# Kernel tuning notes

Measured on AMD Instinct MI355X. Metric: run time of the kernel, lower is better.

The kernel has to match this reference:

```python
import jax, jax.numpy as jnp
import numpy as np

N_NODES = 100000


def gcn_conv(x, edge_index, W, b):
    # PyG GCNConv: add self-loops, symmetric normalization D^-1/2 (A+I) D^-1/2, transform, aggregate, bias.
    src, dst = edge_index[0], edge_index[1]
    n = x.shape[0]
    xw = x @ W  # [N, out] transform before propagate (PyG order)
    # degree with self-loops (count edges by target + 1)
    deg = jax.ops.segment_sum(jnp.ones_like(dst, dtype=xw.dtype), dst, num_segments=n) + 1.0
    dinv = jax.lax.rsqrt(deg)  # deg >= 1, safe
    norm = dinv[src] * dinv[dst]  # [E]
    msgs = xw[src] * norm[:, None]  # [E, out] gathered, normalized messages
    agg = jax.ops.segment_sum(msgs, dst, num_segments=n)
    # self-loop contribution: norm_ii = dinv_i^2 = 1/deg_i
    agg = agg + xw * (dinv * dinv)[:, None]
    return agg + b


def setup_inputs() -> dict:
    key = jax.random.key(0)
    ks = jax.random.split(key, 8)
    in_c, h1, h2, out_c = 128, 71, 82, 1
    x = jax.random.normal(ks[0], (N_NODES, in_c), dtype=jnp.float32)
    edge_index = jax.random.randint(ks[1], (2, 1600000), 0, N_NODES, dtype=jnp.int64)
    def glorot(k, fan_in, fan_out):
        s = jnp.sqrt(6.0 / (fan_in + fan_out))
        return jax.random.uniform(k, (fan_in, fan_out), jnp.float32, -s, s)
    return {
        "x": x,
        "edge_index": edge_index,
        "W1": glorot(ks[2], in_c, h1), "b1": jnp.zeros((h1,), jnp.float32),
        "W2": glorot(ks[3], h1, h2), "b2": jnp.zeros((h2,), jnp.float32),
        "W3": glorot(ks[4], h2, out_c), "b3": jnp.zeros((out_c,), jnp.float32),
    }


def reference(x, edge_index, W1, b1, W2, b2, W3, b3):
    h = jax.nn.relu(gcn_conv(x, edge_index, W1, b1))
    h = gcn_conv(h, edge_index, W2, b2)  # note: no relu after conv2 in source
    return gcn_conv(h, edge_index, W3, b3)
```

## Files before the change

### kernel.cpp

```cpp
#include <hip/hip_runtime.h>
#include <hip/hip_fp16.h>

#define NNODES 100000
#define NB 196
#define BSHIFT 9
#define BMASK 511
#define BCAP 9216
#define WT_LD 136

typedef _Float16 half8 __attribute__((ext_vector_type(8)));
typedef float floatx4 __attribute__((ext_vector_type(4)));

__global__ void binA_kernel(const int* __restrict__ src, const int* __restrict__ dst,
                            int* __restrict__ bcnt, unsigned* __restrict__ bdata, int E) {
    __shared__ int hist[NB];
    __shared__ int gb[NB];
    __shared__ int cur[NB];
    const int BATCH = 4096;
    for (int base = blockIdx.x * BATCH; base < E; base += gridDim.x * BATCH) {
        for (int i = threadIdx.x; i < NB; i += blockDim.x) hist[i] = 0;
        __syncthreads();
        int s[16], d[16];
        int cnt = 0;
        if (base + BATCH <= E) {
#pragma unroll
            for (int q = 0; q < 4; ++q) {
                int4 sv = ((const int4*)(src + base))[q * 256 + threadIdx.x];
                int4 dv = ((const int4*)(dst + base))[q * 256 + threadIdx.x];
                s[cnt] = sv.x; d[cnt] = dv.x; atomicAdd(&hist[dv.x >> BSHIFT], 1); ++cnt;
                s[cnt] = sv.y; d[cnt] = dv.y; atomicAdd(&hist[dv.y >> BSHIFT], 1); ++cnt;
                s[cnt] = sv.z; d[cnt] = dv.z; atomicAdd(&hist[dv.z >> BSHIFT], 1); ++cnt;
                s[cnt] = sv.w; d[cnt] = dv.w; atomicAdd(&hist[dv.w >> BSHIFT], 1); ++cnt;
            }
        } else {
#pragma unroll
            for (int k = 0; k < 16; ++k) {
                int idx = base + k * 256 + threadIdx.x;
                if (idx < E) {
                    s[cnt] = src[idx];
                    d[cnt] = dst[idx];
                    atomicAdd(&hist[d[cnt] >> BSHIFT], 1);
                    ++cnt;
                }
            }
        }
        __syncthreads();
        for (int i = threadIdx.x; i < NB; i += blockDim.x) {
            int c = hist[i];
            gb[i] = (c > 0) ? atomicAdd(&bcnt[i], c) : 0;
            cur[i] = 0;
        }
        __syncthreads();
        for (int k = 0; k < cnt; ++k) {
            int b = d[k] >> BSHIFT;
            int lo = gb[b] + atomicAdd(&cur[b], 1);
            if (lo < BCAP)
                bdata[(size_t)b * BCAP + lo] = ((unsigned)s[k] << BSHIFT) | ((unsigned)d[k] & BMASK);
        }
        __syncthreads();
    }
}

__global__ __launch_bounds__(1024) void prep_kernel(
        const int* __restrict__ bcnt, int* __restrict__ bstart,
        const float* __restrict__ W2, const float* __restrict__ b2,
        const float* __restrict__ W3, float* __restrict__ w23,
        const float* __restrict__ W1, __half* __restrict__ Wt) {
    if (blockIdx.x == 0) {
        __shared__ int sh[NB];
        int t = threadIdx.x;
        if (t < NB) sh[t] = min(bcnt[t], BCAP);
        __syncthreads();
        if (t == 0) {
            int acc = 0;
            for (int i = 0; i < NB; ++i) { int v = sh[i]; sh[i] = acc; acc += v; }
        }
        __syncthreads();
        if (t < NB) bstart[t] = sh[t];
    } else if (blockIdx.x == 1) {
        int k = threadIdx.x;
        if (k < 71) {
            float a = 0.f;
            for (int j = 0; j < 82; ++j) a += W2[k * 82 + j] * W3[j];
            w23[k] = a;
        } else if (k == 71) {
            float a = 0.f;
            for (int j = 0; j < 82; ++j) a += b2[j] * W3[j];
            w23[71] = a;
        }
    } else {
        for (int i = threadIdx.x; i < 80 * WT_LD; i += blockDim.x) {
            int nn = i / WT_LD, k = i - nn * WT_LD;
            float v = (nn < 71 && k < 128) ? W1[k * 71 + nn] : 0.f;
            Wt[i] = __float2half(v);
        }
    }
}

__global__ __launch_bounds__(1024) void binB2_kernel(
        const int* __restrict__ bcnt, const int* __restrict__ bstart,
        const unsigned* __restrict__ bdata,
        int* __restrict__ deg, int* __restrict__ end_off, float* __restrict__ dinv,
        int* __restrict__ csr, int n) {
    __shared__ unsigned edata[BCAP];
    __shared__ int hist[512];
    __shared__ int cur[512];
    __shared__ int wsum[8];
    int b = blockIdx.x;
    int tid = threadIdx.x;
    int cnt = min(bcnt[b], BCAP);
    int base = bstart[b];
    const unsigned* p = bdata + (size_t)b * BCAP;
    if (tid < 512) hist[tid] = 0;
    __syncthreads();
    for (int i = tid; i < cnt; i += 1024) {
        unsigned e = p[i];
        edata[i] = e;
        atomicAdd(&hist[e & BMASK], 1);
    }
    __syncthreads();
    if (tid < 512) {
        int v = hist[tid];
        int lane = tid & 63;
        int incl = v;
#pragma unroll
        for (int off = 1; off < 64; off <<= 1) {
            int t = __shfl_up(incl, off);
            if (lane >= off) incl += t;
        }
        cur[tid] = incl;
        if (lane == 63) wsum[tid >> 6] = incl;
    }
    __syncthreads();
    if (tid == 0) {
        int acc = 0;
#pragma unroll
        for (int w = 0; w < 8; ++w) { int t = wsum[w]; wsum[w] = acc; acc += t; }
    }
    __syncthreads();
    if (tid < 512) {
        int v = hist[tid];
        int start = base + wsum[tid >> 6] + cur[tid] - v;
        int node = (b << BSHIFT) + tid;
        if (node < n) {
            deg[node] = v;
            end_off[node] = start + v;
            dinv[node] = rsqrtf((float)v + 1.0f);
        }
        cur[tid] = start;
    }
    __syncthreads();
    for (int i = tid; i < cnt; i += 1024) {
        unsigned e = edata[i];
        int pos = atomicAdd(&cur[e & BMASK], 1);
        csr[pos] = (int)(e >> BSHIFT);
    }
}

__global__ __launch_bounds__(256) void xform_mfma(
        const float* __restrict__ x, const __half* __restrict__ Wt,
        const float* __restrict__ scale, __half* __restrict__ msgA,
        __half* __restrict__ msgB, int n) {
    __shared__ __half Wsh[80 * WT_LD];
    {
        const uint4* sp = (const uint4*)Wt;
        uint4* dp = (uint4*)Wsh;
        for (int i = threadIdx.x; i < (80 * WT_LD * 2) / 16; i += blockDim.x) dp[i] = sp[i];
    }
    __syncthreads();
    int lane = threadIdx.x & 63;
    int m = lane & 15, q = lane >> 4;
    int gw = (blockIdx.x * blockDim.x + threadIdx.x) >> 6;
    int nw = (gridDim.x * blockDim.x) >> 6;
    int nrt = n >> 4;
    for (int rt = gw; rt < nrt; rt += nw) {
        int rb = rt << 4;
        const float* xr = x + (size_t)(rb + m) * 128 + q * 8;
        floatx4 acc[5];
#pragma unroll
        for (int t = 0; t < 5; ++t) acc[t] = (floatx4){0.f, 0.f, 0.f, 0.f};
#pragma unroll
        for (int ks = 0; ks < 4; ++ks) {
            float4 f0 = *(const float4*)(xr + ks * 32);
            float4 f1 = *(const float4*)(xr + ks * 32 + 4);
            half8 a;
            a[0] = (_Float16)f0.x; a[1] = (_Float16)f0.y;
            a[2] = (_Float16)f0.z; a[3] = (_Float16)f0.w;
            a[4] = (_Float16)f1.x; a[5] = (_Float16)f1.y;
            a[6] = (_Float16)f1.z; a[7] = (_Float16)f1.w;
#pragma unroll
            for (int t = 0; t < 5; ++t) {
                half8 b = *(const half8*)&Wsh[(t * 16 + m) * WT_LD + ks * 32 + q * 8];
                acc[t] = __builtin_amdgcn_mfma_f32_16x16x32_f16(a, b, acc[t], 0, 0, 0);
            }
        }
        float sc[4];
#pragma unroll
        for (int r = 0; r < 4; ++r) sc[r] = scale[rb + q * 4 + r];
#pragma unroll
        for (int t = 0; t < 5; ++t) {
            int col = t * 16 + m;
#pragma unroll
            for (int r = 0; r < 4; ++r) {
                __half hv = __float2half(acc[t][r] * sc[r]);
                int row = rb + q * 4 + r;
                if (t < 4) {
                    msgA[(size_t)row * 64 + col] = hv;
                } else if (m < 8) {
                    msgB[(size_t)row * 8 + m] = hv;
                }
            }
        }
    }
}

__global__ __launch_bounds__(256) void gather_fused(
        const __half* __restrict__ msgA, const __half* __restrict__ msgB,
        const int* __restrict__ csr, const int* __restrict__ end_off,
        const int* __restrict__ deg, const float* __restrict__ dinv,
        const float* __restrict__ b, const float* __restrict__ w23,
        float* __restrict__ g2, int n) {
    int lane = threadIdx.x & 63;
    int li = lane & 7;
    int wid = (blockIdx.x * blockDim.x + threadIdx.x) >> 6;
    int nwaves = (gridDim.x * blockDim.x) >> 6;
    float bA[8], wA[8];
#pragma unroll
    for (int j = 0; j < 8; ++j) { bA[j] = b[8 * li + j]; wA[j] = w23[8 * li + j]; }
    float bB = (li < 7) ? b[64 + li] : 0.f;
    float wB = (li < 7) ? w23[64 + li] : 0.f;
    const char* mA = (const char*)msgA;
    const char* mB = (const char*)msgB;
    unsigned laneA   = (unsigned)(li << 4);
    unsigned laneBof = (unsigned)((li >> 1) << 2);
    unsigned laneBsh = (unsigned)((li & 1) << 4);
    int ntiles = (n + 7) >> 3;
    for (int tile = wid; tile < ntiles; tile += nwaves) {
        int node = (tile << 3) + (lane >> 3);
        int d = -1, st = 0; float dv = 0.f;
        if (node < n) {
            int e = end_off[node];
            d = deg[node];
            st = e - d;
            dv = dinv[node];
        }
        int tmax = d;
        tmax = max(tmax, __shfl_xor(tmax, 8));
        tmax = max(tmax, __shfl_xor(tmax, 16));
        tmax = max(tmax, __shfl_xor(tmax, 32));
        tmax = __builtin_amdgcn_readfirstlane(tmax);
        float acc[8];
#pragma unroll
        for (int j = 0; j < 8; ++j) acc[j] = 0.f;
        float bsum = 0.f;
        int c0 = csr[(0 < d) ? st : 0];
        int c1 = csr[(1 < d) ? st + 1 : 0];
        for (int i = 0; i <= tmax; i += 2) {
            int p0 = csr[(i + 2 < d) ? st + i + 2 : 0];
            int p1 = csr[(i + 3 < d) ? st + i + 3 : 0];
            if (i <= d) {
                unsigned idx = (unsigned)((i < d) ? c0 : node);
                half8 row = *(const half8*)(mA + ((idx << 7) | laneA));
                unsigned bw = *(const unsigned*)(mB + ((idx << 4) | laneBof));
#pragma unroll
                for (int j = 0; j < 8; ++j) acc[j] += (float)row[j];
                unsigned short us = (unsigned short)(bw >> laneBsh);
                _Float16 hf;
                __builtin_memcpy(&hf, &us, 2);
                bsum += (float)hf;
            }
            if (i + 1 <= d) {
                unsigned idx = (unsigned)((i + 1 < d) ? c1 : node);
                half8 row = *(const half8*)(mA + ((idx << 7) | laneA));
                unsigned bw = *(const unsigned*)(mB + ((idx << 4) | laneBof));
#pragma unroll
                for (int j = 0; j < 8; ++j) acc[j] += (float)row[j];
                unsigned short us = (unsigned short)(bw >> laneBsh);
                _Float16 hf;
                __builtin_memcpy(&hf, &us, 2);
                bsum += (float)hf;
            }
            c0 = p0;
            c1 = p1;
        }
        float p = 0.f;
#pragma unroll
        for (int j = 0; j < 8; ++j) p += fmaxf(dv * acc[j] + bA[j], 0.f) * wA[j];
        p += fmaxf(dv * bsum + bB, 0.f) * wB;
        p += __shfl_xor(p, 1);
        p += __shfl_xor(p, 2);
        p += __shfl_xor(p, 4);
        if (node < n && li == 0) g2[node] = dv * p;
    }
}

__global__ void sgather_q(const float* __restrict__ g2, const int* __restrict__ csr,
                          const int* __restrict__ end_off, const int* __restrict__ deg,
                          const float* __restrict__ dinv, const float* __restrict__ w23,
                          float* __restrict__ q, int n) {
    float bw = w23[71];
    int lane = threadIdx.x & 63;
    int g = lane >> 4, k = lane & 15;
    int wid = (blockIdx.x * blockDim.x + threadIdx.x) >> 6;
    int nw = (gridDim.x * blockDim.x) >> 6;
    for (int i0 = wid * 4; i0 < n; i0 += nw * 4) {
        int i = i0 + g;
        float acc = 0.f;
        float dv = 0.f;
        if (i < n) {
            int end = end_off[i];
            int cnt = deg[i];
            int start = end - cnt;
            dv = dinv[i];
            for (int e = k; e < cnt; e += 16) acc += g2[csr[start + e]];
        }
        acc += __shfl_down(acc, 8, 16);
        acc += __shfl_down(acc, 4, 16);
        acc += __shfl_down(acc, 2, 16);
        acc += __shfl_down(acc, 1, 16);
        if (i < n && k == 0) q[i] = dv * (dv * (acc + g2[i]) + bw);
    }
}

__global__ void sgather_out(const float* __restrict__ q, const int* __restrict__ csr,
                            const int* __restrict__ end_off, const int* __restrict__ deg,
                            const float* __restrict__ dinv, const float* __restrict__ b3,
                            float* __restrict__ out, int n) {
    float bv = b3[0];
    int lane = threadIdx.x & 63;
    int g = lane >> 4, k = lane & 15;
    int wid = (blockIdx.x * blockDim.x + threadIdx.x) >> 6;
    int nw = (gridDim.x * blockDim.x) >> 6;
    for (int i0 = wid * 4; i0 < n; i0 += nw * 4) {
        int i = i0 + g;
        float acc = 0.f;
        float dv = 0.f;
        if (i < n) {
            int end = end_off[i];
            int cnt = deg[i];
            int start = end - cnt;
            dv = dinv[i];
            for (int e = k; e < cnt; e += 16) acc += q[csr[start + e]];
        }
        acc += __shfl_down(acc, 8, 16);
        acc += __shfl_down(acc, 4, 16);
        acc += __shfl_down(acc, 2, 16);
        acc += __shfl_down(acc, 1, 16);
        if (i < n && k == 0) out[i] = dv * (acc + q[i]) + bv;
    }
}

extern "C" void kernel_launch(void* const* d_in, const int* in_sizes, int n_in,
                              void* d_out, int out_size, void* d_ws, size_t ws_size,
                              hipStream_t stream) {
    const float* x  = (const float*)d_in[0];
    const int*   ei = (const int*)d_in[1];
    const float* W1 = (const float*)d_in[2];
    const float* b1 = (const float*)d_in[3];
    const float* W2 = (const float*)d_in[4];
    const float* b2 = (const float*)d_in[5];
    const float* W3 = (const float*)d_in[6];
    const float* b3 = (const float*)d_in[7];
    float* out = (float*)d_out;

    const int n = NNODES;
    const int E = in_sizes[1] / 2;
    const int* src = ei;
    const int* dst = ei + E;

    float* ws     = (float*)d_ws;
    float* dinv   = ws;
    int*   deg_i  = (int*)(ws + n);
    int*   offs   = deg_i + n;
    int*   bcnt   = offs + n;
    int*   bstart = bcnt + 256;
    float* w23    = (float*)(bstart + 256);
    __half* Wt    = (__half*)(w23 + 80);
    float* g2     = (float*)(Wt + 11008);
    float* q      = g2 + n;
    int*   csr    = (int*)(q + n);
    __half* msgA  = (__half*)(csr + E + 16);
    __half* msgB  = msgA + (size_t)n * 64;
    unsigned* bdata = (unsigned*)(msgB + (size_t)n * 8);

    hipMemsetAsync(bcnt, 0, 256 * sizeof(int), stream);
    binA_kernel<<<(E + 4095) / 4096, 256, 0, stream>>>(src, dst, bcnt, bdata, E);
    prep_kernel<<<3, 1024, 0, stream>>>(bcnt, bstart, W2, b2, W3, w23, W1, Wt);
    binB2_kernel<<<NB, 1024, 0, stream>>>(bcnt, bstart, bdata, deg_i, offs, dinv, csr, n);

    xform_mfma<<<1563, 256, 0, stream>>>(x, Wt, dinv, msgA, msgB, n);

    gather_fused<<<1563, 256, 0, stream>>>(msgA, msgB, csr, offs, deg_i, dinv, b1, w23, g2, n);

    sgather_q<<<1024, 256, 0, stream>>>(g2, csr, offs, deg_i, dinv, w23, q, n);
    sgather_out<<<1024, 256, 0, stream>>>(q, csr, offs, deg_i, dinv, b3, out, n);
}
```

Before: 225.7 us.

## Software-pipeline layer-1 gather with fdot2 accumulation, finer bins, larger grids

The layer-1 gather now keeps 16 outstanding row loads in flight with explicit double-buffered issue/consume stages and scheduling barriers. It accumulates half pairs via fdot2 and uses a zero sentinel row instead of per-edge predication. Binning switches to 256-node buckets across more blocks, the scalar gathers unroll by two, and grids double. These are meant to hide gather latency and raise parallelism, at the cost of higher register pressure and extra padded iterations for low-degree tiles.

```diff
diff --git a/kernel.cpp b/kernel.cpp
--- a/kernel.cpp
+++ b/kernel.cpp
@@ -2,13 +2,14 @@
 #include <hip/hip_fp16.h>
 
 #define NNODES 100000
-#define NB 196
-#define BSHIFT 9
-#define BMASK 511
-#define BCAP 9216
+#define NB 391
+#define BSHIFT 8
+#define BMASK 255
+#define BCAP 4864
 #define WT_LD 136
 
 typedef _Float16 half8 __attribute__((ext_vector_type(8)));
+typedef _Float16 half2_t __attribute__((ext_vector_type(2)));
 typedef float floatx4 __attribute__((ext_vector_type(4)));
 
 __global__ void binA_kernel(const int* __restrict__ src, const int* __restrict__ dst,
@@ -103,15 +104,15 @@
         int* __restrict__ deg, int* __restrict__ end_off, float* __restrict__ dinv,
         int* __restrict__ csr, int n) {
     __shared__ unsigned edata[BCAP];
-    __shared__ int hist[512];
-    __shared__ int cur[512];
-    __shared__ int wsum[8];
+    __shared__ int hist[256];
+    __shared__ int cur[256];
+    __shared__ int wsum[4];
     int b = blockIdx.x;
     int tid = threadIdx.x;
     int cnt = min(bcnt[b], BCAP);
     int base = bstart[b];
     const unsigned* p = bdata + (size_t)b * BCAP;
-    if (tid < 512) hist[tid] = 0;
+    if (tid < 256) hist[tid] = 0;
     __syncthreads();
     for (int i = tid; i < cnt; i += 1024) {
         unsigned e = p[i];
@@ -119,7 +120,7 @@
         atomicAdd(&hist[e & BMASK], 1);
     }
     __syncthreads();
-    if (tid < 512) {
+    if (tid < 256) {
         int v = hist[tid];
         int lane = tid & 63;
         int incl = v;
@@ -135,10 +136,10 @@
     if (tid == 0) {
         int acc = 0;
 #pragma unroll
-        for (int w = 0; w < 8; ++w) { int t = wsum[w]; wsum[w] = acc; acc += t; }
-    }
-    __syncthreads();
-    if (tid < 512) {
+        for (int w = 0; w < 4; ++w) { int t = wsum[w]; wsum[w] = acc; acc += t; }
+    }
+    __syncthreads();
+    if (tid < 256) {
         int v = hist[tid];
         int start = base + wsum[tid >> 6] + cur[tid] - v;
         int node = (b << BSHIFT) + tid;
@@ -214,83 +215,135 @@
     }
 }
 
+
+#define CONS(RR, WW) do { \
+    half2_t p0_ = {RR[0], RR[1]}, p1_ = {RR[2], RR[3]}; \
+    half2_t p2_ = {RR[4], RR[5]}, p3_ = {RR[6], RR[7]}; \
+    a0 = __builtin_amdgcn_fdot2(p0_, H10, a0, false); \
+    a1 = __builtin_amdgcn_fdot2(p0_, H01, a1, false); \
+    a2 = __builtin_amdgcn_fdot2(p1_, H10, a2, false); \
+    a3 = __builtin_amdgcn_fdot2(p1_, H01, a3, false); \
+    a4 = __builtin_amdgcn_fdot2(p2_, H10, a4, false); \
+    a5 = __builtin_amdgcn_fdot2(p2_, H01, a5, false); \
+    a6 = __builtin_amdgcn_fdot2(p3_, H10, a6, false); \
+    a7 = __builtin_amdgcn_fdot2(p3_, H01, a7, false); \
+    half2_t wv_; __builtin_memcpy(&wv_, &(WW), 4); \
+    bsum = __builtin_amdgcn_fdot2(wv_, HB, bsum, false); \
+} while (0)
+
+#define ISSUE(S, C, RR, WW, S2) do { \
+    unsigned idx_ = ((S) < d) ? (unsigned)(C) : ZR; \
+    RR = *(const half8*)(mA + (((size_t)idx_ << 7) | laneA)); \
+    WW = *(const unsigned*)(mB + (((size_t)idx_ << 4) | laneBof)); \
+    C = csr[((S2) < d) ? st + (S2) : 0]; \
+} while (0)
+
+#define PISSUE(S, CV, RR, WW) do { \
+    unsigned idx_ = ((S) < d) ? (unsigned)(CV) : ZR; \
+    RR = *(const half8*)(mA + (((size_t)idx_ << 7) | laneA)); \
+    WW = *(const unsigned*)(mB + (((size_t)idx_ << 4) | laneBof)); \
+} while (0)
+
+#define CSRP(S) csr[((S) < d) ? st + (S) : 0]
+
 __global__ __launch_bounds__(256) void gather_fused(
         const __half* __restrict__ msgA, const __half* __restrict__ msgB,
         const int* __restrict__ csr, const int* __restrict__ end_off,
         const int* __restrict__ deg, const float* __restrict__ dinv,
         const float* __restrict__ b, const float* __restrict__ w23,
         float* __restrict__ g2, int n) {
+    const unsigned ZR = (unsigned)NNODES;
+    const half2_t H10 = {(_Float16)1.f, (_Float16)0.f};
+    const half2_t H01 = {(_Float16)0.f, (_Float16)1.f};
     int lane = threadIdx.x & 63;
     int li = lane & 7;
+    const half2_t HB = (li & 1) ? H01 : H10;
     int wid = (blockIdx.x * blockDim.x + threadIdx.x) >> 6;
     int nwaves = (gridDim.x * blockDim.x) >> 6;
-    float bA[8], wA[8];
-#pragma unroll
-    for (int j = 0; j < 8; ++j) { bA[j] = b[8 * li + j]; wA[j] = w23[8 * li + j]; }
-    float bB = (li < 7) ? b[64 + li] : 0.f;
-    float wB = (li < 7) ? w23[64 + li] : 0.f;
     const char* mA = (const char*)msgA;
     const char* mB = (const char*)msgB;
     unsigned laneA   = (unsigned)(li << 4);
     unsigned laneBof = (unsigned)((li >> 1) << 2);
-    unsigned laneBsh = (unsigned)((li & 1) << 4);
-    int ntiles = (n + 7) >> 3;
+    int ntiles = n >> 3;
     for (int tile = wid; tile < ntiles; tile += nwaves) {
         int node = (tile << 3) + (lane >> 3);
-        int d = -1, st = 0; float dv = 0.f;
-        if (node < n) {
-            int e = end_off[node];
-            d = deg[node];
-            st = e - d;
-            dv = dinv[node];
-        }
+        int ee = end_off[node];
+        int d = deg[node];
+        int st = ee - d;
+        float dv = dinv[node];
         int tmax = d;
         tmax = max(tmax, __shfl_xor(tmax, 8));
         tmax = max(tmax, __shfl_xor(tmax, 16));
         tmax = max(tmax, __shfl_xor(tmax, 32));
         tmax = __builtin_amdgcn_readfirstlane(tmax);
-        float acc[8];
-#pragma unroll
-        for (int j = 0; j < 8; ++j) acc[j] = 0.f;
-        float bsum = 0.f;
-        int c0 = csr[(0 < d) ? st : 0];
-        int c1 = csr[(1 < d) ? st + 1 : 0];
-        for (int i = 0; i <= tmax; i += 2) {
-            int p0 = csr[(i + 2 < d) ? st + i + 2 : 0];
-            int p1 = csr[(i + 3 < d) ? st + i + 3 : 0];
-            if (i <= d) {
-                unsigned idx = (unsigned)((i < d) ? c0 : node);
-                half8 row = *(const half8*)(mA + ((idx << 7) | laneA));
-                unsigned bw = *(const unsigned*)(mB + ((idx << 4) | laneBof));
-#pragma unroll
-                for (int j = 0; j < 8; ++j) acc[j] += (float)row[j];
-                unsigned short us = (unsigned short)(bw >> laneBsh);
-                _Float16 hf;
-                __builtin_memcpy(&hf, &us, 2);
-                bsum += (float)hf;
-            }
-            if (i + 1 <= d) {
-                unsigned idx = (unsigned)((i + 1 < d) ? c1 : node);
-                half8 row = *(const half8*)(mA + ((idx << 7) | laneA));
-                unsigned bw = *(const unsigned*)(mB + ((idx << 4) | laneBof));
-#pragma unroll
-                for (int j = 0; j < 8; ++j) acc[j] += (float)row[j];
-                unsigned short us = (unsigned short)(bw >> laneBsh);
-                _Float16 hf;
-                __builtin_memcpy(&hf, &us, 2);
-                bsum += (float)hf;
-            }
-            c0 = p0;
-            c1 = p1;
-        }
+        int tmaxr = (tmax + 15) & ~15;
+        float a0, a1, a2, a3, a4, a5, a6, a7, bsum;
+        {
+            half8 sr = *(const half8*)(mA + (((size_t)(unsigned)node << 7) | laneA));
+            unsigned sw = *(const unsigned*)(mB + (((size_t)(unsigned)node << 4) | laneBof));
+            a0 = (float)sr[0]; a1 = (float)sr[1]; a2 = (float)sr[2]; a3 = (float)sr[3];
+            a4 = (float)sr[4]; a5 = (float)sr[5]; a6 = (float)sr[6]; a7 = (float)sr[7];
+            half2_t wv; __builtin_memcpy(&wv, &sw, 4);
+            bsum = __builtin_amdgcn_fdot2(wv, HB, 0.f, false);
+        }
+        int k0 = CSRP(0),  k1 = CSRP(1),  k2 = CSRP(2),  k3 = CSRP(3);
+        int k4 = CSRP(4),  k5 = CSRP(5),  k6 = CSRP(6),  k7 = CSRP(7);
+        int k8 = CSRP(8),  k9 = CSRP(9),  k10 = CSRP(10), k11 = CSRP(11);
+        int k12 = CSRP(12), k13 = CSRP(13), k14 = CSRP(14), k15 = CSRP(15);
+        int ca0 = CSRP(16), ca1 = CSRP(17), ca2 = CSRP(18), ca3 = CSRP(19);
+        int ca4 = CSRP(20), ca5 = CSRP(21), ca6 = CSRP(22), ca7 = CSRP(23);
+        int cb0 = CSRP(24), cb1 = CSRP(25), cb2 = CSRP(26), cb3 = CSRP(27);
+        int cb4 = CSRP(28), cb5 = CSRP(29), cb6 = CSRP(30), cb7 = CSRP(31);
+        half8 ra0, ra1, ra2, ra3, ra4, ra5, ra6, ra7;
+        half8 rb0, rb1, rb2, rb3, rb4, rb5, rb6, rb7;
+        unsigned wa0, wa1, wa2, wa3, wa4, wa5, wa6, wa7;
+        unsigned wb0, wb1, wb2, wb3, wb4, wb5, wb6, wb7;
+        PISSUE(0, k0, ra0, wa0);  PISSUE(1, k1, ra1, wa1);
+        PISSUE(2, k2, ra2, wa2);  PISSUE(3, k3, ra3, wa3);
+        PISSUE(4, k4, ra4, wa4);  PISSUE(5, k5, ra5, wa5);
+        PISSUE(6, k6, ra6, wa6);  PISSUE(7, k7, ra7, wa7);
+        PISSUE(8, k8, rb0, wb0);  PISSUE(9, k9, rb1, wb1);
+        PISSUE(10, k10, rb2, wb2); PISSUE(11, k11, rb3, wb3);
+        PISSUE(12, k12, rb4, wb4); PISSUE(13, k13, rb5, wb5);
+        PISSUE(14, k14, rb6, wb6); PISSUE(15, k15, rb7, wb7);
+        for (int i = 0; i < tmaxr; i += 16) {
+            CONS(ra0, wa0); CONS(ra1, wa1); CONS(ra2, wa2); CONS(ra3, wa3);
+            CONS(ra4, wa4); CONS(ra5, wa5); CONS(ra6, wa6); CONS(ra7, wa7);
+            __builtin_amdgcn_sched_barrier(0);
+            ISSUE(i + 16, ca0, ra0, wa0, i + 32);
+            ISSUE(i + 17, ca1, ra1, wa1, i + 33);
+            ISSUE(i + 18, ca2, ra2, wa2, i + 34);
+            ISSUE(i + 19, ca3, ra3, wa3, i + 35);
+            ISSUE(i + 20, ca4, ra4, wa4, i + 36);
+            ISSUE(i + 21, ca5, ra5, wa5, i + 37);
+            ISSUE(i + 22, ca6, ra6, wa6, i + 38);
+            ISSUE(i + 23, ca7, ra7, wa7, i + 39);
+            __builtin_amdgcn_sched_barrier(0);
+            CONS(rb0, wb0); CONS(rb1, wb1); CONS(rb2, wb2); CONS(rb3, wb3);
+            CONS(rb4, wb4); CONS(rb5, wb5); CONS(rb6, wb6); CONS(rb7, wb7);
+            __builtin_amdgcn_sched_barrier(0);
+            ISSUE(i + 24, cb0, rb0, wb0, i + 40);
+            ISSUE(i + 25, cb1, rb1, wb1, i + 41);
+            ISSUE(i + 26, cb2, rb2, wb2, i + 42);
+            ISSUE(i + 27, cb3, rb3, wb3, i + 43);
+            ISSUE(i + 28, cb4, rb4, wb4, i + 44);
+            ISSUE(i + 29, cb5, rb5, wb5, i + 45);
+            ISSUE(i + 30, cb6, rb6, wb6, i + 46);
+            ISSUE(i + 31, cb7, rb7, wb7, i + 47);
+            __builtin_amdgcn_sched_barrier(0);
+        }
+        float av[8] = {a0, a1, a2, a3, a4, a5, a6, a7};
         float p = 0.f;
 #pragma unroll
-        for (int j = 0; j < 8; ++j) p += fmaxf(dv * acc[j] + bA[j], 0.f) * wA[j];
+        for (int j = 0; j < 8; ++j)
+            p += fmaxf(dv * av[j] + b[8 * li + j], 0.f) * w23[8 * li + j];
+        float bB = (li < 7) ? b[64 + li] : 0.f;
+        float wB = (li < 7) ? w23[64 + li] : 0.f;
         p += fmaxf(dv * bsum + bB, 0.f) * wB;
         p += __shfl_xor(p, 1);
         p += __shfl_xor(p, 2);
         p += __shfl_xor(p, 4);
-        if (node < n && li == 0) g2[node] = dv * p;
+        if (li == 0) g2[node] = dv * p;
     }
 }
 
@@ -312,7 +365,13 @@
             int cnt = deg[i];
             int start = end - cnt;
             dv = dinv[i];
-            for (int e = k; e < cnt; e += 16) acc += g2[csr[start + e]];
+            int e = k;
+            for (; e + 16 < cnt; e += 32) {
+                int a0 = csr[start + e];
+                int a1 = csr[start + e + 16];
+                acc += g2[a0] + g2[a1];
+            }
+            for (; e < cnt; e += 16) acc += g2[csr[start + e]];
         }
         acc += __shfl_down(acc, 8, 16);
         acc += __shfl_down(acc, 4, 16);
@@ -340,7 +399,13 @@
             int cnt = deg[i];
             int start = end - cnt;
             dv = dinv[i];
-            for (int e = k; e < cnt; e += 16) acc += q[csr[start + e]];
+            int e = k;
+            for (; e + 16 < cnt; e += 32) {
+                int a0 = csr[start + e];
+                int a1 = csr[start + e + 16];
+                acc += q[a0] + q[a1];
+            }
+            for (; e < cnt; e += 16) acc += q[csr[start + e]];
         }
         acc += __shfl_down(acc, 8, 16);
         acc += __shfl_down(acc, 4, 16);
@@ -373,25 +438,27 @@
     int*   deg_i  = (int*)(ws + n);
     int*   offs   = deg_i + n;
     int*   bcnt   = offs + n;
-    int*   bstart = bcnt + 256;
-    float* w23    = (float*)(bstart + 256);
+    int*   bstart = bcnt + 512;
+    float* w23    = (float*)(bstart + 512);
     __half* Wt    = (__half*)(w23 + 80);
     float* g2     = (float*)(Wt + 11008);
     float* q      = g2 + n;
     int*   csr    = (int*)(q + n);
     __half* msgA  = (__half*)(csr + E + 16);
-    __half* msgB  = msgA + (size_t)n * 64;
-    unsigned* bdata = (unsigned*)(msgB + (size_t)n * 8);
-
-    hipMemsetAsync(bcnt, 0, 256 * sizeof(int), stream);
+    __half* msgB  = msgA + (size_t)(n + 8) * 64;
+    unsigned* bdata = (unsigned*)(msgB + (size_t)(n + 8) * 8);
+
+    hipMemsetAsync(bcnt, 0, 512 * sizeof(int), stream);
+    hipMemsetAsync(msgA + (size_t)n * 64, 0, 64 * sizeof(__half), stream);
+    hipMemsetAsync(msgB + (size_t)n * 8, 0, 8 * sizeof(__half), stream);
     binA_kernel<<<(E + 4095) / 4096, 256, 0, stream>>>(src, dst, bcnt, bdata, E);
     prep_kernel<<<3, 1024, 0, stream>>>(bcnt, bstart, W2, b2, W3, w23, W1, Wt);
     binB2_kernel<<<NB, 1024, 0, stream>>>(bcnt, bstart, bdata, deg_i, offs, dinv, csr, n);
 
     xform_mfma<<<1563, 256, 0, stream>>>(x, Wt, dinv, msgA, msgB, n);
 
-    gather_fused<<<1563, 256, 0, stream>>>(msgA, msgB, csr, offs, deg_i, dinv, b1, w23, g2, n);
-
-    sgather_q<<<1024, 256, 0, stream>>>(g2, csr, offs, deg_i, dinv, w23, q, n);
-    sgather_out<<<1024, 256, 0, stream>>>(q, csr, offs, deg_i, dinv, b3, out, n);
-}
+    gather_fused<<<3125, 256, 0, stream>>>(msgA, msgB, csr, offs, deg_i, dinv, b1, w23, g2, n);
+
+    sgather_q<<<2048, 256, 0, stream>>>(g2, csr, offs, deg_i, dinv, w23, q, n);
+    sgather_out<<<2048, 256, 0, stream>>>(q, csr, offs, deg_i, dinv, b3, out, n);
+}
```

Result: no change. 225.0 us (-0.3%).
